# Optimization experiments

Hardware: AMD Instinct MI355X
Metric: run time of the kernel (lower is better)

## Reference

```python
import jax, jax.numpy as jnp
import numpy as np

INPUT_SIZE = 1024
HIDDEN_SIZE = 1024

def _xavier(key, shape):
    fan_in, fan_out = shape
    limit = np.sqrt(6.0 / (fan_in + fan_out))
    return jax.random.uniform(key, shape, jnp.float32, -limit, limit)

def setup_inputs() -> dict:
    key = jax.random.key(0)
    ks = jax.random.split(key, 9)
    x = jax.random.normal(ks[0], (64, 512, INPUT_SIZE), jnp.float32)
    d = {"x": x}
    names_i = ["W_ii", "W_fi", "W_gi", "W_oi"]
    names_h = ["W_ih", "W_fh", "W_gh", "W_oh"]
    for n, k in zip(names_i, ks[1:5]):
        d[n] = _xavier(k, (INPUT_SIZE, HIDDEN_SIZE))
    for n, k in zip(names_h, ks[5:9]):
        d[n] = _xavier(k, (HIDDEN_SIZE, HIDDEN_SIZE))
    for n in ["b_ii", "b_ih", "b_fi", "b_fh", "b_gi", "b_gh", "b_oi", "b_oh"]:
        d[n] = jnp.zeros((HIDDEN_SIZE,), jnp.float32)
    return d

def _lstm(x, W_ii, W_ih, b_ii, b_ih, W_fi, W_fh, b_fi, b_fh,
          W_gi, W_gh, b_gi, b_gh, W_oi, W_oh, b_oi, b_oh):
    B, S, _ = x.shape
    H = W_ih.shape[0]
    # Fuse the 4 input-side GEMMs into one and hoist out of the recurrence.
    Wi = jnp.concatenate([W_ii, W_fi, W_gi, W_oi], axis=1)          # [I, 4H]
    Wh = jnp.concatenate([W_ih, W_fh, W_gh, W_oh], axis=1)          # [H, 4H]
    bi = jnp.concatenate([b_ii + b_ih, b_fi + b_fh, b_gi + b_gh, b_oi + b_oh])
    xproj = jnp.einsum('bsi,ig->bsg', x, Wi) + bi                    # [B, S, 4H]

    def step(carry, xp_t):
        h, c = carry
        gates = xp_t + h @ Wh                                        # [B, 4H]
        i_t = jax.nn.sigmoid(gates[:, 0 * H:1 * H])
        f_t = jax.nn.sigmoid(gates[:, 1 * H:2 * H])
        g_t = jnp.tanh(gates[:, 2 * H:3 * H])
        o_t = jax.nn.sigmoid(gates[:, 3 * H:4 * H])
        c = f_t * c + i_t * g_t
        h = o_t * jnp.tanh(c)
        return (h, c), None

    h0 = jnp.zeros((B, H), x.dtype)
    c0 = jnp.zeros((B, H), x.dtype)
    (h_t, c_t), _ = jax.lax.scan(step, (h0, c0), jnp.swapaxes(xproj, 0, 1))
    return h_t, c_t

def reference(x, W_ii, W_ih, b_ii, b_ih, W_fi, W_fh, b_fi, b_fh,
              W_gi, W_gh, b_gi, b_gh, W_oi, W_oh, b_oi, b_oh):
    return _lstm(x, W_ii, W_ih, b_ii, b_ih, W_fi, W_fh, b_fi, b_fh,
                 W_gi, W_gh, b_gi, b_gh, W_oi, W_oh, b_oi, b_oh)
```

## Files before the change

kernel.cpp:

```cpp
#include <hip/hip_runtime.h>
#include <hip/hip_bf16.h>

#define SEQ   512
#define HID   1024
#define NBLK  256
#define NTHR  256
#define PADK  2056
#define GPS   36

typedef __attribute__((ext_vector_type(8))) short bf16x8;
typedef __attribute__((ext_vector_type(4))) float f32x4;
typedef __attribute__((ext_vector_type(2))) float f32x2;

struct Params {
  const float* x;
  const float* Wi[4];
  const float* Wh[4];
  const float* bi[4];
  const float* bh[4];
  float* out;
  const short* xbf;
  short* hb0;
  short* hb1;
  unsigned* arrive;
  unsigned* gen;
};

__device__ __forceinline__ float sig_(float v)  { return 1.0f / (1.0f + __expf(-v)); }
__device__ __forceinline__ float tanh_(float v) { return 1.0f - 2.0f / (__expf(2.0f * v) + 1.0f); }

__device__ __forceinline__ short f2b(float f) {
  unsigned u = __builtin_bit_cast(unsigned, f);
  u += 0x7FFFu + ((u >> 16) & 1u);
  return (short)(u >> 16);
}
__device__ __forceinline__ bf16x8 cvt8(const float* p) {
  f32x4 a = *(const f32x4*)p;
  f32x4 b = *(const f32x4*)(p + 4);
  bf16x8 r;
  r[0] = f2b(a[0]); r[1] = f2b(a[1]); r[2] = f2b(a[2]); r[3] = f2b(a[3]);
  r[4] = f2b(b[0]); r[5] = f2b(b[1]); r[6] = f2b(b[2]); r[7] = f2b(b[3]);
  return r;
}

__device__ __forceinline__ bf16x8 ld16_sc1(const short* p) {
  bf16x8 r;
  asm volatile("global_load_dwordx4 %0, %1, off sc1" : "=v"(r) : "v"(p));
  return r;
}
__device__ __forceinline__ void wait_vm0() {
  asm volatile("s_waitcnt vmcnt(0)" ::: "memory");
}

__global__ __launch_bounds__(256) void init_ws(unsigned* bar, unsigned* hzero, int hn) {
  int i = blockIdx.x * blockDim.x + threadIdx.x;
  if (i < 8448) bar[i] = 0u;
  if (i < hn) hzero[i] = 0u;
}

__global__ __launch_bounds__(256) void cvt_x(const float* __restrict__ x,
                                             short* __restrict__ xb) {
  size_t i = ((size_t)blockIdx.x * 256 + threadIdx.x) * 8;
  *(bf16x8*)(xb + i) = cvt8(x + i);
}

__device__ __forceinline__ void gbar_fence(unsigned* arrive, unsigned* gen,
                                           int tid, int bid, unsigned tgt) {
  __syncthreads();
  if (bid == 0) {
    if (tid != 0) {
      int polls = 0;
      while (__hip_atomic_load(&arrive[tid * 32], __ATOMIC_RELAXED,
                               __HIP_MEMORY_SCOPE_AGENT) < tgt) {
        __builtin_amdgcn_s_sleep(1);
        if (++polls > (1 << 22)) break;
      }
    }
    __syncthreads();
    if (tid == 0) {
      __threadfence();
      __hip_atomic_store(gen, tgt, __ATOMIC_RELEASE, __HIP_MEMORY_SCOPE_AGENT);
    }
    __syncthreads();
  } else {
    if (tid == 0) {
      __threadfence();
      __hip_atomic_store(&arrive[bid * 32], tgt, __ATOMIC_RELEASE,
                         __HIP_MEMORY_SCOPE_AGENT);
      int polls = 0;
      while (__hip_atomic_load(gen, __ATOMIC_RELAXED,
                               __HIP_MEMORY_SCOPE_AGENT) < tgt) {
        __builtin_amdgcn_s_sleep(1);
        if (++polls > (1 << 22)) break;
      }
      __threadfence();
    }
    __syncthreads();
  }
}

template <bool FULL>
__global__ __launch_bounds__(NTHR, 1) void lstm_persistent(Params p) {
  extern __shared__ char smem[];
  short* bls    = (short*)smem;
  float* gparts = (float*)(smem + 131584);
  float* cst    = (float*)(smem + 131584 + 18432);
  float* bias_s = (float*)(smem + 131584 + 18432 + 1024);

  const int tid = threadIdx.x;
  const int bid = blockIdx.x;
  const int cg  = bid & 127;
  const int mh  = bid >> 7;
  const int r0  = mh * 32;
  const int j0  = cg * 8;

  {
    const int g    = tid & 3;
    const int krow = tid >> 2;
    const float* wi = p.Wi[g];
    const float* wh = p.Wh[g];
    for (int kb = 0; kb < 2048; kb += 64) {
      int k = kb + krow;
      const float* src = (k < HID) ? (wi + (size_t)k * HID + j0)
                                   : (wh + (size_t)(k - HID) * HID + j0);
      f32x4 va = *(const f32x4*)src;
      f32x4 vb = *(const f32x4*)(src + 4);
      #pragma unroll
      for (int jj = 0; jj < 4; ++jj) {
        bls[(4 * jj + g) * PADK + k]       = f2b(va[jj]);
        bls[(4 * (jj + 4) + g) * PADK + k] = f2b(vb[jj]);
      }
    }
  }
  if (tid < 32) {
    int g = tid & 3, j = j0 + (tid >> 2);
    bias_s[tid] = p.bi[g][j] + p.bh[g][j];
  }
  if (tid < 128) { cst[2 * tid] = 0.0f; cst[2 * tid + 1] = 0.0f; }
  __syncthreads();

  const int lane = tid & 63;
  const int ksl  = tid >> 6;
  const int m16  = lane & 15;
  const int quad = lane >> 4;
  const size_t rm0 = (size_t)(r0 + m16);
  const size_t rm1 = (size_t)(r0 + 16 + m16);
  const short* bB0 = bls + (size_t)m16 * PADK + ksl * 512 + quad * 8;
  const short* bB1 = bls + (size_t)(16 + m16) * PADK + ksl * 512 + quad * 8;

  float cfin0 = 0.0f, cfin1 = 0.0f;

  for (int t = 0; t < SEQ; ++t) {
    f32x4 acc00 = {0,0,0,0}, acc01 = {0,0,0,0};
    f32x4 acc10 = {0,0,0,0}, acc11 = {0,0,0,0};

    if constexpr (FULL) {
      if (ksl < 2) {
        const short* xb = p.xbf + ksl * 512 + quad * 8 + (size_t)t * HID;
        const short* pa0 = xb + rm0 * (SEQ * HID);
        const short* pa1 = xb + rm1 * (SEQ * HID);
        #pragma unroll 4
        for (int ki = 0; ki < 16; ++ki) {
          bf16x8 a0 = *(const bf16x8*)(pa0 + ki * 32);
          bf16x8 a1 = *(const bf16x8*)(pa1 + ki * 32);
          bf16x8 b0 = *(const bf16x8*)(bB0 + ki * 32);
          bf16x8 b1 = *(const bf16x8*)(bB1 + ki * 32);
          acc00 = __builtin_amdgcn_mfma_f32_16x16x32_bf16(a0, b0, acc00, 0, 0, 0);
          acc01 = __builtin_amdgcn_mfma_f32_16x16x32_bf16(a0, b1, acc01, 0, 0, 0);
          acc10 = __builtin_amdgcn_mfma_f32_16x16x32_bf16(a1, b0, acc10, 0, 0, 0);
          acc11 = __builtin_amdgcn_mfma_f32_16x16x32_bf16(a1, b1, acc11, 0, 0, 0);
        }
      } else {
        const short* hr = ((t & 1) ? p.hb1 : p.hb0) + (ksl - 2) * 512 + quad * 8;
        const short* pa0 = hr + rm0 * HID;
        const short* pa1 = hr + rm1 * HID;
        bf16x8 A0[16], A1[16];
        #pragma unroll
        for (int ki = 0; ki < 16; ++ki) {
          A0[ki] = ld16_sc1(pa0 + ki * 32);
          A1[ki] = ld16_sc1(pa1 + ki * 32);
        }
        wait_vm0();
        #pragma unroll
        for (int ki = 0; ki < 16; ++ki) {
          asm volatile("" : "+v"(A0[ki]));
          asm volatile("" : "+v"(A1[ki]));
        }
        #pragma unroll
        for (int ki = 0; ki < 16; ++ki) {
          bf16x8 b0 = *(const bf16x8*)(bB0 + ki * 32);
          bf16x8 b1 = *(const bf16x8*)(bB1 + ki * 32);
          acc00 = __builtin_amdgcn_mfma_f32_16x16x32_bf16(A0[ki], b0, acc00, 0, 0, 0);
          acc01 = __builtin_amdgcn_mfma_f32_16x16x32_bf16(A0[ki], b1, acc01, 0, 0, 0);
          acc10 = __builtin_amdgcn_mfma_f32_16x16x32_bf16(A1[ki], b0, acc10, 0, 0, 0);
          acc11 = __builtin_amdgcn_mfma_f32_16x16x32_bf16(A1[ki], b1, acc11, 0, 0, 0);
        }
      }
    } else {
      const float *fa0, *fa1;
      if (ksl < 2) {
        const float* xb = p.x + ksl * 512 + quad * 8 + (size_t)t * HID;
        fa0 = xb + rm0 * (SEQ * HID);
        fa1 = xb + rm1 * (SEQ * HID);
      } else {
        const float* hr = (p.out + ((t & 1) ? 65536 : 0)) + (ksl - 2) * 512 + quad * 8;
        fa0 = hr + rm0 * HID;
        fa1 = hr + rm1 * HID;
      }
      #pragma unroll 2
      for (int ki = 0; ki < 16; ++ki) {
        bf16x8 a0 = cvt8(fa0 + ki * 32);
        bf16x8 a1 = cvt8(fa1 + ki * 32);
        bf16x8 b0 = *(const bf16x8*)(bB0 + ki * 32);
        bf16x8 b1 = *(const bf16x8*)(bB1 + ki * 32);
        acc00 = __builtin_amdgcn_mfma_f32_16x16x32_bf16(a0, b0, acc00, 0, 0, 0);
        acc01 = __builtin_amdgcn_mfma_f32_16x16x32_bf16(a0, b1, acc01, 0, 0, 0);
        acc10 = __builtin_amdgcn_mfma_f32_16x16x32_bf16(a1, b0, acc10, 0, 0, 0);
        acc11 = __builtin_amdgcn_mfma_f32_16x16x32_bf16(a1, b1, acc11, 0, 0, 0);
      }
    }

    {
      float* gp = gparts + ksl * (32 * GPS);
      #pragma unroll
      for (int r = 0; r < 4; ++r) {
        gp[(quad * 4 + r) * GPS + m16]           = acc00[r];
        gp[(quad * 4 + r) * GPS + 16 + m16]      = acc01[r];
        gp[(16 + quad * 4 + r) * GPS + m16]      = acc10[r];
        gp[(16 + quad * 4 + r) * GPS + 16 + m16] = acc11[r];
      }
    }
    __syncthreads();

    if (tid < 128) {
      int rl = tid >> 2, jp = tid & 3;
      f32x4 ga = {0,0,0,0}, gb = {0,0,0,0};
      #pragma unroll
      for (int s = 0; s < 4; ++s) {
        const float* gp = gparts + s * (32 * GPS) + rl * GPS + jp * 8;
        ga += *(const f32x4*)gp;
        gb += *(const f32x4*)(gp + 4);
      }
      f32x4 ba = *(const f32x4*)(bias_s + jp * 8);
      f32x4 bb = *(const f32x4*)(bias_s + jp * 8 + 4);

      float i0 = sig_(ga[0] + ba[0]);
      float f0 = sig_(ga[1] + ba[1]);
      float g0 = tanh_(ga[2] + ba[2]);
      float o0 = sig_(ga[3] + ba[3]);
      float i1 = sig_(gb[0] + bb[0]);
      float f1 = sig_(gb[1] + bb[1]);
      float g1 = tanh_(gb[2] + bb[2]);
      float o1 = sig_(gb[3] + bb[3]);

      int ci = rl * 8 + jp * 2;
      float c0 = f0 * cst[ci]     + i0 * g0;
      float c1 = f1 * cst[ci + 1] + i1 * g1;
      cst[ci] = c0; cst[ci + 1] = c1;
      float h0v = o0 * tanh_(c0);
      float h1v = o1 * tanh_(c1);

      size_t off = (size_t)(r0 + rl) * HID + j0 + jp * 2;
      if constexpr (FULL) {
        short* hw = (t & 1) ? p.hb0 : p.hb1;
        unsigned u = (unsigned)(unsigned short)f2b(h0v) |
                     ((unsigned)(unsigned short)f2b(h1v) << 16);
        __hip_atomic_store((unsigned*)(hw + off), u, __ATOMIC_RELAXED,
                           __HIP_MEMORY_SCOPE_AGENT);
        if (t == SEQ - 1) {
          f32x2 hv = {h0v, h1v}; *(f32x2*)(p.out + off) = hv;
          f32x2 cv = {c0, c1};   *(f32x2*)(p.out + 65536 + off) = cv;
        }
      } else {
        float* hw = p.out + ((t & 1) ? 0 : 65536);
        f32x2 hv = {h0v, h1v};
        *(f32x2*)(hw + off) = hv;
        if (t == SEQ - 1) { cfin0 = c0; cfin1 = c1; }
      }
    }

    if (t < SEQ - 1) {
      if constexpr (FULL) {
        unsigned tgt = (unsigned)(t + 1);
        __syncthreads();
        if (bid == 0) {
          if (tid != 0) {
            int polls = 0;
            while (__hip_atomic_load(&p.arrive[tid * 32], __ATOMIC_RELAXED,
                                     __HIP_MEMORY_SCOPE_AGENT) < tgt) {
              __builtin_amdgcn_s_sleep(2);
              if (++polls > (1 << 22)) break;
            }
          }
          __syncthreads();
          if (tid == 0)
            __hip_atomic_store(p.gen, tgt, __ATOMIC_RELAXED,
                               __HIP_MEMORY_SCOPE_AGENT);
          __syncthreads();
        } else {
          if (tid == 0) {
            __hip_atomic_store(&p.arrive[bid * 32], tgt, __ATOMIC_RELAXED,
                               __HIP_MEMORY_SCOPE_AGENT);
            int polls = 0;
            while (__hip_atomic_load(p.gen, __ATOMIC_RELAXED,
                                     __HIP_MEMORY_SCOPE_AGENT) < tgt) {
              __builtin_amdgcn_s_sleep(2);
              if (++polls > (1 << 22)) break;
            }
          }
          __syncthreads();
        }
      } else {
        gbar_fence(p.arrive, p.gen, tid, bid, (unsigned)(t + 1));
      }
    }
  }

  if constexpr (!FULL) {
    if (tid < 128) {
      int rl = tid >> 2, jp = tid & 3;
      size_t off = (size_t)(r0 + rl) * HID + j0 + jp * 2;
      f32x2 cv = {cfin0, cfin1};
      *(f32x2*)(p.out + 65536 + off) = cv;
    }
  }
}

extern "C" void kernel_launch(void* const* d_in, const int* in_sizes, int n_in,
                              void* d_out, int out_size, void* d_ws, size_t ws_size,
                              hipStream_t stream) {
  Params prm;
  prm.x = (const float*)d_in[0];
  for (int g = 0; g < 4; ++g) {
    prm.Wi[g] = (const float*)d_in[1 + g];
    prm.Wh[g] = (const float*)d_in[5 + g];
    prm.bi[g] = (const float*)d_in[9 + 2 * g];
    prm.bh[g] = (const float*)d_in[10 + 2 * g];
  }
  prm.out    = (float*)d_out;
  prm.arrive = (unsigned*)d_ws;
  prm.gen    = prm.arrive + 8192;
  prm.xbf = nullptr; prm.hb0 = nullptr; prm.hb1 = nullptr;

  const size_t need_full = 65536 + 67108864 + 2 * 131072;
  const bool full = ws_size >= need_full;
  if (full) {
    prm.xbf = (const short*)((char*)d_ws + 65536);
    prm.hb0 = (short*)((char*)d_ws + 65536 + 67108864);
    prm.hb1 = prm.hb0 + 65536;
  }

  const int smem_bytes = 131584 + 18432 + 1024 + 128;
  hipFuncSetAttribute((const void*)lstm_persistent<true>,
                      hipFuncAttributeMaxDynamicSharedMemorySize, smem_bytes);
  hipFuncSetAttribute((const void*)lstm_persistent<false>,
                      hipFuncAttributeMaxDynamicSharedMemorySize, smem_bytes);

  if (full) {
    init_ws<<<256, 256, 0, stream>>>((unsigned*)d_ws, (unsigned*)prm.hb0, 32768);
    cvt_x<<<16384, 256, 0, stream>>>(prm.x, (short*)prm.xbf);
    lstm_persistent<true><<<NBLK, NTHR, smem_bytes, stream>>>(prm);
  } else {
    init_ws<<<256, 256, 0, stream>>>((unsigned*)d_ws, (unsigned*)d_out, 65536);
    lstm_persistent<false><<<NBLK, NTHR, smem_bytes, stream>>>(prm);
  }
}
```

Before: 4.164 ms.

## Replace centralized grid barrier with per-producer flag polling in recurrent waves

Drops the two-level grid barrier, where block 0 gathered arrivals and broadcast a generation counter. Each block now publishes its step counter in its own arrive slot, and each h-reading lane polls only the flag of the producer block it depends on before loading h. This removes the broadcast round trip and lets blocks proceed as soon as their specific inputs are ready. The risk is memory-ordering correctness, since relaxed atomics carry no explicit fence, and the mapping from lanes to producer blocks must exactly match which block writes which h rows.

```diff
diff --git a/kernel.cpp b/kernel.cpp
--- a/kernel.cpp
+++ b/kernel.cpp
@@ -148,6 +148,9 @@
   const short* bB0 = bls + (size_t)m16 * PADK + ksl * 512 + quad * 8;
   const short* bB1 = bls + (size_t)(16 + m16) * PADK + ksl * 512 + quad * 8;
 
+  const unsigned* myflag =
+      p.arrive + (size_t)(mh * 128 + (ksl - 2) * 64 + lane) * 32;
+
   float cfin0 = 0.0f, cfin1 = 0.0f;
 
   for (int t = 0; t < SEQ; ++t) {
@@ -171,6 +174,14 @@
           acc11 = __builtin_amdgcn_mfma_f32_16x16x32_bf16(a1, b1, acc11, 0, 0, 0);
         }
       } else {
+        if (t > 0) {
+          int polls = 0;
+          while (__hip_atomic_load(myflag, __ATOMIC_RELAXED,
+                                   __HIP_MEMORY_SCOPE_AGENT) < (unsigned)t) {
+            __builtin_amdgcn_s_sleep(1);
+            if (++polls > (1 << 22)) break;
+          }
+        }
         const short* hr = ((t & 1) ? p.hb1 : p.hb0) + (ksl - 2) * 512 + quad * 8;
         const short* pa0 = hr + rm0 * HID;
         const short* pa1 = hr + rm1 * HID;
@@ -279,40 +290,14 @@
       }
     }
 
-    if (t < SEQ - 1) {
-      if constexpr (FULL) {
-        unsigned tgt = (unsigned)(t + 1);
-        __syncthreads();
-        if (bid == 0) {
-          if (tid != 0) {
-            int polls = 0;
-            while (__hip_atomic_load(&p.arrive[tid * 32], __ATOMIC_RELAXED,
-                                     __HIP_MEMORY_SCOPE_AGENT) < tgt) {
-              __builtin_amdgcn_s_sleep(2);
-              if (++polls > (1 << 22)) break;
-            }
-          }
-          __syncthreads();
-          if (tid == 0)
-            __hip_atomic_store(p.gen, tgt, __ATOMIC_RELAXED,
-                               __HIP_MEMORY_SCOPE_AGENT);
-          __syncthreads();
-        } else {
-          if (tid == 0) {
-            __hip_atomic_store(&p.arrive[bid * 32], tgt, __ATOMIC_RELAXED,
-                               __HIP_MEMORY_SCOPE_AGENT);
-            int polls = 0;
-            while (__hip_atomic_load(p.gen, __ATOMIC_RELAXED,
-                                     __HIP_MEMORY_SCOPE_AGENT) < tgt) {
-              __builtin_amdgcn_s_sleep(2);
-              if (++polls > (1 << 22)) break;
-            }
-          }
-          __syncthreads();
-        }
-      } else {
+    if constexpr (FULL) {
+      __syncthreads();
+      if (t < SEQ - 1 && tid == 0)
+        __hip_atomic_store(&p.arrive[bid * 32], (unsigned)(t + 1),
+                           __ATOMIC_RELAXED, __HIP_MEMORY_SCOPE_AGENT);
+    } else {
+      if (t < SEQ - 1)
         gbar_fence(p.arrive, p.gen, tid, bid, (unsigned)(t + 1));
-      }
     }
   }
 
```

Result: faster. 3.687 ms (-11.4%).
